# Optimization experiments

Measured on AMD Instinct MI355X. Metric: run time of the kernel, lower is better.

## Reference

```python
import jax, jax.numpy as jnp
import numpy as np

B, D_IN, D_HID, D_OUT = 16384, 256, 512, 256
E, K = 8, 2  # expert_num, activate_num


def setup_inputs() -> dict:
    key = jax.random.key(0)
    ks = jax.random.split(key, 6)
    s_in = 1.0 / np.sqrt(D_IN)
    s_hid = 1.0 / np.sqrt(D_HID)
    return {
        "x": jax.random.normal(ks[0], (B, D_IN), dtype=jnp.float32),
        "Wg": jax.random.normal(ks[1], (D_IN, E), dtype=jnp.float32) * s_in,
        "W1": jax.random.normal(ks[2], (E, D_IN, D_HID), dtype=jnp.float32) * s_in,
        "b1": jnp.zeros((E, D_HID), dtype=jnp.float32),
        "W2": jax.random.normal(ks[3], (E, D_HID, D_OUT), dtype=jnp.float32) * s_hid,
        "b2": jnp.zeros((E, D_OUT), dtype=jnp.float32),
    }


def reference(x, Wg, W1, b1, W2, b2):
    # Gating: logits -> top-k -> softmax over the k selected logits.
    # (nn.Dropout on gate logits is identity at inference.)
    gate_logits = x @ Wg                              # [B, E]
    weights, selected = jax.lax.top_k(gate_logits, K)  # [B, K], [B, K]
    weights = jax.nn.softmax(weights.astype(jnp.float32), axis=1).astype(x.dtype)

    # Expert compute, vectorized over experts (same math as the per-expert
    # gather/compute/scatter loop; tokens not routed to expert e get weight 0).
    h = jax.nn.relu(jnp.einsum("bd,edh->ebh", x, W1) + b1[:, None, :])  # [E, B, H]
    expert_out = jnp.einsum("ebh,eho->ebo", h, W2) + b2[:, None, :]      # [E, B, O]

    # Combine weights: combine[b, e] = sum_k weights[b,k] * [selected[b,k]==e]
    one_hot = jax.nn.one_hot(selected, E, dtype=x.dtype)  # [B, K, E]
    combine = jnp.einsum("bk,bke->be", weights, one_hot)  # [B, E]
    results = jnp.einsum("be,ebo->bo", combine, expert_out)  # [B, O]
    return results
```

## Files before the change

kernel.cpp:

```cpp
#include <hip/hip_runtime.h>
#include <hip/hip_bf16.h>

typedef __bf16 bf16x8 __attribute__((ext_vector_type(8)));
typedef __bf16 bf16x4 __attribute__((ext_vector_type(4)));
typedef float f32x4 __attribute__((ext_vector_type(4)));
typedef float f32x16 __attribute__((ext_vector_type(16)));

#define NTOK 16384
#define DIN  256
#define DHID 512
#define DOUT 256
#define NEXP 8

#define MFMA32(a, b, c) __builtin_amdgcn_mfma_f32_32x32x16_bf16(a, b, c, 0, 0, 0)
#define GLD16(gp, lp)                                                       \
  __builtin_amdgcn_global_load_lds(                                         \
      (__attribute__((address_space(1))) void*)(gp),                        \
      (__attribute__((address_space(3))) void*)(lp), 16, 0, 0)

__global__ __launch_bounds__(256) void prep_kernel(
    const float* __restrict__ x, const float* __restrict__ wg,
    const float* __restrict__ w1, const float* __restrict__ w2,
    int* __restrict__ cnt, int* __restrict__ btok, float* __restrict__ bw,
    __bf16* __restrict__ xbf, __bf16* __restrict__ w1bf,
    __bf16* __restrict__ w2bf) {
  __shared__ int lcnt[NEXP];
  __shared__ int lbase[NEXP];
  const int b = blockIdx.x;
  const int tid = threadIdx.x;

  if (b >= 512) {
    if (b < 1024) {
      int e = (b - 512) >> 6;
      int flat = ((b - 512) & 63) * 256 + tid;
      int kg = flat >> 9;
      int n = flat & 511;
      const float* s = w1 + ((size_t)e * 256 + (size_t)kg * 8) * 512 + n;
      bf16x8 t;
#pragma unroll
      for (int j = 0; j < 8; ++j) t[j] = (__bf16)s[(size_t)j * 512];
      *(bf16x8*)(w1bf + (size_t)(e * 512 + n) * 256 + kg * 8) = t;
    } else {
      int e = (b - 1024) >> 6;
      int flat = ((b - 1024) & 63) * 256 + tid;
      int kg = flat >> 8;
      int n = flat & 255;
      const float* s = w2 + ((size_t)e * 512 + (size_t)kg * 8) * 256 + n;
      bf16x8 t;
#pragma unroll
      for (int j = 0; j < 8; ++j) t[j] = (__bf16)s[(size_t)j * 256];
      *(bf16x8*)(w2bf + (size_t)(e * 256 + n) * 512 + kg * 8) = t;
    }
    return;
  }

  if (tid < NEXP) lcnt[tid] = 0;

  const int sub = tid & 7;
  const int tslot = tid >> 3;
  const int token = b * 32 + tslot;
  const f32x4* xr = (const f32x4*)(x + (size_t)token * DIN + sub * 32);
  const float* wr0 = wg + (size_t)sub * 32 * NEXP;

  bf16x8 xb[4];
  f32x4 p0 = {0.f, 0.f, 0.f, 0.f}, p1 = {0.f, 0.f, 0.f, 0.f};
#pragma unroll
  for (int j4 = 0; j4 < 8; ++j4) {
    f32x4 xv = xr[j4];
    const float* wr = wr0 + j4 * 32;
#pragma unroll
    for (int d = 0; d < 4; ++d) {
      float xs_ = xv[d];
      p0 += xs_ * *(const f32x4*)(wr + 8 * d);
      p1 += xs_ * *(const f32x4*)(wr + 8 * d + 4);
      xb[j4 >> 1][(j4 & 1) * 4 + d] = (__bf16)xs_;
    }
  }
  {
    bf16x8* xdst = (bf16x8*)(xbf + (size_t)token * DIN + sub * 32);
#pragma unroll
    for (int i = 0; i < 4; ++i) xdst[i] = xb[i];
  }

  double acc[NEXP];
#pragma unroll
  for (int d = 0; d < 4; ++d) {
    acc[d] = (double)p0[d];
    acc[4 + d] = (double)p1[d];
  }
#pragma unroll
  for (int off = 1; off < 8; off <<= 1)
#pragma unroll
    for (int e = 0; e < NEXP; ++e) acc[e] += __shfl_xor(acc[e], off, 64);

  __syncthreads();

  int i1 = 0, i2 = 0, o1 = 0, o2 = 0;
  float w1s = 0.f, w2s = 0.f;
  if (sub == 0) {
    double bv1 = acc[0];
#pragma unroll
    for (int e = 1; e < NEXP; ++e)
      if (acc[e] > bv1) { bv1 = acc[e]; i1 = e; }
    double bv2 = -1e300;
#pragma unroll
    for (int e = 0; e < NEXP; ++e)
      if (e != i1 && acc[e] > bv2) { bv2 = acc[e]; i2 = e; }
    float dd = expf((float)(bv2 - bv1));
    w1s = 1.0f / (1.0f + dd);
    w2s = dd * w1s;
    o1 = atomicAdd(&lcnt[i1], 1);
    o2 = atomicAdd(&lcnt[i2], 1);
  }
  __syncthreads();
  if (tid < NEXP) lbase[tid] = atomicAdd(&cnt[tid], lcnt[tid]);
  __syncthreads();
  if (sub == 0) {
    int s1 = lbase[i1] + o1, s2 = lbase[i2] + o2;
    btok[i1 * NTOK + s1] = token;
    bw[i1 * NTOK + s1] = w1s;
    btok[i2 * NTOK + s2] = token | 16384;
    bw[i2 * NTOK + s2] = w2s;
  }
}

__global__ __launch_bounds__(256, 2) void ffn_kernel(
    const __bf16* __restrict__ xbf, const __bf16* __restrict__ w1bf,
    const __bf16* __restrict__ w2bf, const float* __restrict__ b1g,
    const float* __restrict__ b2g, const int* __restrict__ cnt,
    const int* __restrict__ btok, const float* __restrict__ bw,
    __bf16* __restrict__ pout) {
  __shared__ __align__(16) __bf16 wb1[64 * 256];
  __shared__ __align__(16) __bf16 wb2[256 * 64];
  __shared__ __align__(16) __bf16 hs[64 * 64];
  __shared__ int tok[64];
  __shared__ int srow[64];
  __shared__ float wgt[64];
  __shared__ float b2s[DOUT];

  int b = blockIdx.x;
  int e = -1, start = 0;
  {
    int a0 = 0;
#pragma unroll
    for (int q = 0; q < NEXP; ++q) {
      int t = (cnt[q] + 63) >> 6;
      if (e < 0 && b < a0 + t) { e = q; start = (b - a0) * 64; }
      a0 += t;
    }
  }
  if (e < 0) return;
  const int ce = cnt[e];
  const int rot = (blockIdx.x >> 3) & 7;

  const int tid = threadIdx.x;
  if (tid < 64) {
    int idx = start + tid;
    bool v = idx < ce;
    int entry = v ? btok[e * NTOK + idx] : 0;
    int tk = entry & 16383;
    tok[tid] = tk;
    srow[tid] = (entry >> 14) * NTOK + tk;
    wgt[tid] = v ? bw[e * NTOK + idx] : 0.0f;
  }
  b2s[tid] = b2g[e * DOUT + tid];
  __syncthreads();

  const int lane = tid & 63;
  const int wid = tid >> 6;
  const int hi = lane >> 5;
  const int l31 = lane & 31;
  const int wh = wid >> 1;
  const int wt = wid & 1;
  const int wo = wid;

  bf16x8 xB[16];
  {
    const __bf16* xr = xbf + (size_t)tok[wt * 32 + l31] * DIN + hi * 8;
#pragma unroll
    for (int kw = 0; kw < 16; ++kw) xB[kw] = *(const bf16x8*)(xr + kw * 16);
  }

  const __bf16* w1e = w1bf + (size_t)e * DHID * DIN;
  const __bf16* w2e = w2bf + (size_t)e * DOUT * DHID;

  f32x16 acc[2][2];
#pragma unroll
  for (int ai = 0; ai < 2; ++ai)
#pragma unroll
    for (int bi = 0; bi < 2; ++bi)
#pragma unroll
      for (int r = 0; r < 16; ++r) acc[ai][bi][r] = 0.f;

  for (int hc0 = 0; hc0 < 8; ++hc0) {
    const int hc = (hc0 + rot) & 7;
    __syncthreads();

#pragma unroll
    for (int j = 0; j < 8; ++j) {
      int W = wid * 8 + j;
      int n1 = 2 * W + hi;
      int s1 = l31 ^ (n1 & 31);
      GLD16(w1e + (size_t)(hc * 64 + n1) * DIN + s1 * 8, wb1 + W * 512);
      int n2 = 8 * W + (lane >> 3);
      int s2 = (lane & 7) ^ (n2 & 7);
      GLD16(w2e + (size_t)n2 * DHID + hc * 64 + s2 * 8, wb2 + W * 512);
    }
    __syncthreads();

    f32x16 Sp[2];
#pragma unroll
    for (int r = 0; r < 16; ++r) { Sp[0][r] = 0.f; Sp[1][r] = 0.f; }
#pragma unroll
    for (int kw = 0; kw < 16; ++kw) {
      int row = wh * 32 + l31;
      int s = (kw * 2 + hi) ^ (row & 31);
      bf16x8 a = *(const bf16x8*)((const char*)wb1 + row * 512 + s * 16);
      Sp[kw & 1] = MFMA32(a, xB[kw], Sp[kw & 1]);
    }
    f32x16 S = Sp[0] + Sp[1];
#pragma unroll
    for (int g = 0; g < 4; ++g) {
      int hl = wh * 32 + 8 * g + 4 * hi;
      f32x4 bv = *(const f32x4*)(b1g + e * DHID + hc * 64 + hl);
      bf16x4 pk;
#pragma unroll
      for (int r = 0; r < 4; ++r)
        pk[r] = (__bf16)fmaxf(S[4 * g + r] + bv[r], 0.f);
      int m = wt * 32 + l31;
      int slt = (hl >> 3) ^ (m & 7);
      *(bf16x4*)((char*)hs + m * 128 + slt * 16 + (hl & 7) * 2) = pk;
    }
    __syncthreads();

#pragma unroll
    for (int kw = 0; kw < 4; ++kw) {
      bf16x8 wf[2], hf[2];
#pragma unroll
      for (int ai = 0; ai < 2; ++ai) {
        int row = wo * 64 + ai * 32 + l31;
        int s = (kw * 2 + hi) ^ (row & 7);
        wf[ai] = *(const bf16x8*)((const char*)wb2 + row * 128 + s * 16);
      }
#pragma unroll
      for (int bi = 0; bi < 2; ++bi) {
        int m = bi * 32 + l31;
        int s = (kw * 2 + hi) ^ (m & 7);
        hf[bi] = *(const bf16x8*)((const char*)hs + m * 128 + s * 16);
      }
      acc[0][0] = MFMA32(wf[0], hf[0], acc[0][0]);
      acc[0][1] = MFMA32(wf[0], hf[1], acc[0][1]);
      acc[1][0] = MFMA32(wf[1], hf[0], acc[1][0]);
      acc[1][1] = MFMA32(wf[1], hf[1], acc[1][1]);
    }
  }

#pragma unroll
  for (int bi = 0; bi < 2; ++bi) {
    int tm = bi * 32 + l31;
    if (start + tm < ce) {
      float wv = wgt[tm];
      __bf16* prow = pout + (size_t)srow[tm] * DOUT;
#pragma unroll
      for (int ai = 0; ai < 2; ++ai) {
#pragma unroll
        for (int g = 0; g < 4; ++g) {
          int o0 = wo * 64 + ai * 32 + 8 * g + 4 * hi;
          f32x4 bv = *(const f32x4*)(&b2s[o0]);
          bf16x4 pk;
#pragma unroll
          for (int r = 0; r < 4; ++r)
            pk[r] = (__bf16)(wv * (acc[ai][bi][4 * g + r] + bv[r]));
          *(bf16x4*)(prow + o0) = pk;
        }
      }
    }
  }
}

__global__ __launch_bounds__(256) void combine_kernel(const __bf16* __restrict__ pout,
                                                      float* __restrict__ out) {
  int f = blockIdx.x * 256 + threadIdx.x;
  bf16x8 a = *(const bf16x8*)(pout + (size_t)f * 8);
  bf16x8 b = *(const bf16x8*)(pout + (size_t)NTOK * DOUT + (size_t)f * 8);
  float4 o0, o1;
  o0.x = (float)a[0] + (float)b[0];
  o0.y = (float)a[1] + (float)b[1];
  o0.z = (float)a[2] + (float)b[2];
  o0.w = (float)a[3] + (float)b[3];
  o1.x = (float)a[4] + (float)b[4];
  o1.y = (float)a[5] + (float)b[5];
  o1.z = (float)a[6] + (float)b[6];
  o1.w = (float)a[7] + (float)b[7];
  float4* dst = (float4*)(out + (size_t)f * 8);
  dst[0] = o0;
  dst[1] = o1;
}

extern "C" void kernel_launch(void* const* d_in, const int* in_sizes, int n_in,
                              void* d_out, int out_size, void* d_ws, size_t ws_size,
                              hipStream_t stream) {
  const float* x = (const float*)d_in[0];
  const float* Wg = (const float*)d_in[1];
  const float* W1 = (const float*)d_in[2];
  const float* b1 = (const float*)d_in[3];
  const float* W2 = (const float*)d_in[4];
  const float* b2 = (const float*)d_in[5];
  float* out = (float*)d_out;

  char* ws = (char*)d_ws;
  int* cnt = (int*)(ws + 0);
  int* btok = (int*)(ws + 256);
  float* bw = (float*)(ws + 524544);
  __bf16* xbf = (__bf16*)(ws + 1048832);
  __bf16* w1bf = (__bf16*)(ws + 9437440);
  __bf16* w2bf = (__bf16*)(ws + 11534592);
  __bf16* pout = (__bf16*)(ws + 13631744);

  hipMemsetAsync(cnt, 0, NEXP * sizeof(int), stream);

  prep_kernel<<<dim3(1536), dim3(256), 0, stream>>>(x, Wg, W1, W2, cnt, btok,
                                                    bw, xbf, w1bf, w2bf);
  ffn_kernel<<<dim3(520), dim3(256), 0, stream>>>(xbf, w1bf, w2bf, b1, b2,
                                                  cnt, btok, bw, pout);
  combine_kernel<<<dim3(NTOK * DOUT / 8 / 256), dim3(256), 0, stream>>>(pout, out);
}
```

Baseline: 159.3 us.

## Double-buffer W1 in LDS and load W2 fragments directly into registers

The prep kernel now writes W2 in a fragment-ordered layout so each wave can load its MFMA A-operands straight from global memory into registers, which removes the W2 staging buffer from LDS. W1 tiles are double-buffered in LDS, and the next chunk is prefetched while the current one is computed. Manual vmcnt waits and raw s_barrier replace __syncthreads, and b1 is cached in LDS. The code relies on exact vmcnt counting, which is fragile, and it raises register pressure from holding 8 W2 fragments per wave.

```diff
diff --git a/kernel.cpp b/kernel.cpp
--- a/kernel.cpp
+++ b/kernel.cpp
@@ -42,14 +42,20 @@
       *(bf16x8*)(w1bf + (size_t)(e * 512 + n) * 256 + kg * 8) = t;
     } else {
       int e = (b - 1024) >> 6;
-      int flat = ((b - 1024) & 63) * 256 + tid;
-      int kg = flat >> 8;
-      int n = flat & 255;
-      const float* s = w2 + ((size_t)e * 512 + (size_t)kg * 8) * 256 + n;
+      int fi = ((b - 1024) & 63) * 256 + tid;
+      int l31v = fi & 31;
+      int hiv = (fi >> 5) & 1;
+      int kwv = (fi >> 6) & 3;
+      int aiv = (fi >> 8) & 1;
+      int wov = (fi >> 9) & 3;
+      int hcv = (fi >> 11) & 7;
+      int hid0 = hcv * 64 + kwv * 16 + hiv * 8;
+      int o = wov * 64 + aiv * 32 + l31v;
+      const float* s = w2 + ((size_t)e * 512 + hid0) * 256 + o;
       bf16x8 t;
 #pragma unroll
       for (int j = 0; j < 8; ++j) t[j] = (__bf16)s[(size_t)j * 256];
-      *(bf16x8*)(w2bf + (size_t)(e * 256 + n) * 512 + kg * 8) = t;
+      *(bf16x8*)(w2bf + (size_t)e * 131072 + (size_t)fi * 8) = t;
     }
     return;
   }
@@ -130,13 +136,13 @@
     const float* __restrict__ b2g, const int* __restrict__ cnt,
     const int* __restrict__ btok, const float* __restrict__ bw,
     __bf16* __restrict__ pout) {
-  __shared__ __align__(16) __bf16 wb1[64 * 256];
-  __shared__ __align__(16) __bf16 wb2[256 * 64];
+  __shared__ __align__(16) __bf16 wb1[2][64 * 256];
   __shared__ __align__(16) __bf16 hs[64 * 64];
   __shared__ int tok[64];
   __shared__ int srow[64];
   __shared__ float wgt[64];
   __shared__ float b2s[DOUT];
+  __shared__ float b1s[DHID];
 
   int b = blockIdx.x;
   int e = -1, start = 0;
@@ -164,6 +170,8 @@
     wgt[tid] = v ? bw[e * NTOK + idx] : 0.0f;
   }
   b2s[tid] = b2g[e * DOUT + tid];
+  b1s[tid] = b1g[e * DHID + tid];
+  b1s[tid + 256] = b1g[e * DHID + tid + 256];
   __syncthreads();
 
   const int lane = tid & 63;
@@ -192,21 +200,45 @@
 #pragma unroll
       for (int r = 0; r < 16; ++r) acc[ai][bi][r] = 0.f;
 
+#define STAGE_W1(bufidx, hcv)                                               \
+  {                                                                         \
+    _Pragma("unroll")                                                       \
+    for (int j = 0; j < 8; ++j) {                                           \
+      int W = wid * 8 + j;                                                  \
+      int n1 = 2 * W + hi;                                                  \
+      int s1 = l31 ^ (n1 & 31);                                             \
+      GLD16(w1e + (size_t)((hcv) * 64 + n1) * DIN + s1 * 8,                 \
+            &wb1[bufidx][W * 512]);                                         \
+    }                                                                       \
+  }
+
+  STAGE_W1(0, rot);
+
+#pragma unroll
   for (int hc0 = 0; hc0 < 8; ++hc0) {
     const int hc = (hc0 + rot) & 7;
-    __syncthreads();
-
-#pragma unroll
-    for (int j = 0; j < 8; ++j) {
-      int W = wid * 8 + j;
-      int n1 = 2 * W + hi;
-      int s1 = l31 ^ (n1 & 31);
-      GLD16(w1e + (size_t)(hc * 64 + n1) * DIN + s1 * 8, wb1 + W * 512);
-      int n2 = 8 * W + (lane >> 3);
-      int s2 = (lane & 7) ^ (n2 & 7);
-      GLD16(w2e + (size_t)n2 * DHID + hc * 64 + s2 * 8, wb2 + W * 512);
-    }
-    __syncthreads();
+    const int cur = hc0 & 1;
+
+    bf16x8 wfr[8];
+    {
+      const __bf16* w2t = w2e + ((size_t)(hc * 4 + wo) << 12);
+#pragma unroll
+      for (int j = 0; j < 8; ++j)
+        wfr[j] = *(const bf16x8*)(w2t + j * 512 + lane * 8);
+    }
+    __builtin_amdgcn_sched_barrier(0);
+    if (hc0 < 7) {
+      STAGE_W1(cur ^ 1, (hc0 + 1 + rot) & 7);
+    }
+    __builtin_amdgcn_sched_barrier(0);
+    if (hc0 < 7) {
+      asm volatile("s_waitcnt vmcnt(16)" ::: "memory");
+    } else {
+      asm volatile("s_waitcnt vmcnt(8)" ::: "memory");
+    }
+    __builtin_amdgcn_sched_barrier(0);
+    __builtin_amdgcn_s_barrier();
+    __builtin_amdgcn_sched_barrier(0);
 
     f32x16 Sp[2];
 #pragma unroll
@@ -215,14 +247,14 @@
     for (int kw = 0; kw < 16; ++kw) {
       int row = wh * 32 + l31;
       int s = (kw * 2 + hi) ^ (row & 31);
-      bf16x8 a = *(const bf16x8*)((const char*)wb1 + row * 512 + s * 16);
+      bf16x8 a = *(const bf16x8*)((const char*)&wb1[cur][0] + row * 512 + s * 16);
       Sp[kw & 1] = MFMA32(a, xB[kw], Sp[kw & 1]);
     }
     f32x16 S = Sp[0] + Sp[1];
 #pragma unroll
     for (int g = 0; g < 4; ++g) {
       int hl = wh * 32 + 8 * g + 4 * hi;
-      f32x4 bv = *(const f32x4*)(b1g + e * DHID + hc * 64 + hl);
+      f32x4 bv = *(const f32x4*)(&b1s[hc * 64 + hl]);
       bf16x4 pk;
 #pragma unroll
       for (int r = 0; r < 4; ++r)
@@ -231,29 +263,27 @@
       int slt = (hl >> 3) ^ (m & 7);
       *(bf16x4*)((char*)hs + m * 128 + slt * 16 + (hl & 7) * 2) = pk;
     }
-    __syncthreads();
+    asm volatile("s_waitcnt lgkmcnt(0)" ::: "memory");
+    __builtin_amdgcn_sched_barrier(0);
+    __builtin_amdgcn_s_barrier();
+    __builtin_amdgcn_sched_barrier(0);
 
 #pragma unroll
     for (int kw = 0; kw < 4; ++kw) {
-      bf16x8 wf[2], hf[2];
-#pragma unroll
-      for (int ai = 0; ai < 2; ++ai) {
-        int row = wo * 64 + ai * 32 + l31;
-        int s = (kw * 2 + hi) ^ (row & 7);
-        wf[ai] = *(const bf16x8*)((const char*)wb2 + row * 128 + s * 16);
-      }
+      bf16x8 hf[2];
 #pragma unroll
       for (int bi = 0; bi < 2; ++bi) {
         int m = bi * 32 + l31;
         int s = (kw * 2 + hi) ^ (m & 7);
         hf[bi] = *(const bf16x8*)((const char*)hs + m * 128 + s * 16);
       }
-      acc[0][0] = MFMA32(wf[0], hf[0], acc[0][0]);
-      acc[0][1] = MFMA32(wf[0], hf[1], acc[0][1]);
-      acc[1][0] = MFMA32(wf[1], hf[0], acc[1][0]);
-      acc[1][1] = MFMA32(wf[1], hf[1], acc[1][1]);
-    }
-  }
+      acc[0][0] = MFMA32(wfr[0 * 4 + kw], hf[0], acc[0][0]);
+      acc[0][1] = MFMA32(wfr[0 * 4 + kw], hf[1], acc[0][1]);
+      acc[1][0] = MFMA32(wfr[1 * 4 + kw], hf[0], acc[1][0]);
+      acc[1][1] = MFMA32(wfr[1 * 4 + kw], hf[1], acc[1][1]);
+    }
+  }
+#undef STAGE_W1
 
 #pragma unroll
   for (int bi = 0; bi < 2; ++bi) {
```

Measured after the change: 157.5 us. About the same (-1.1%).
